# Performance work log

Hardware: AMD Instinct MI355X
Metric: run time of the kernel (lower is better)

## Reference

```python
import jax, jax.numpy as jnp
import numpy as np

N_SAMPLES = 10
DROPOUT_P = 0.1
EPS = 1e-12
B, F, C = 32768, 512, 1000


def setup_inputs() -> dict:
    key = jax.random.key(0)
    k1, k2, k3, k4 = jax.random.split(key, 4)
    return {
        "features": jax.random.normal(k1, (B, F), dtype=jnp.float32),
        "logits": jax.random.normal(k2, (B, C), dtype=jnp.float32),
        "W": jax.random.normal(k3, (F, C), dtype=jnp.float32) * 0.05,
        "b": jax.random.normal(k4, (C,), dtype=jnp.float32) * 0.05,
    }


def reference(features, logits, W, b):
    # `logits` is part of the provider interface but unused by this provider.
    del logits
    keep_p = 1.0 - DROPOUT_P
    mask_key = jax.random.key(42)
    # (n_samples, batch, feat) Bernoulli keep masks; inverted-dropout scaling.
    masks = jax.random.bernoulli(mask_key, keep_p, (N_SAMPLES,) + features.shape)
    dropped = jnp.where(masks, features[None] / keep_p, 0.0)  # (S, B, F)
    lgts = jnp.einsum("sbf,fc->sbc", dropped, W) + b          # (S, B, C)
    probs = jax.nn.softmax(lgts, axis=-1)                      # (S, B, C)
    mean = jnp.mean(probs, axis=0)                             # (B, C)
    # torch .var(dim=0) uses unbiased (n-1) normalization.
    var = jnp.sum((probs - mean[None]) ** 2, axis=0) / (N_SAMPLES - 1)
    total_var = jnp.sum(var, axis=-1, keepdims=True)           # (B, 1)
    # Scaler not fitted -> _normalize is identity.
    return jnp.log(total_var + EPS)
```

## Files before the change

kernel.cpp:

```cpp
#include <hip/hip_runtime.h>
#include <hip/hip_bf16.h>
#include <stdint.h>
#include <math.h>

typedef __attribute__((ext_vector_type(8))) short short8;
typedef __attribute__((ext_vector_type(4))) float f32x4;

namespace {
constexpr int kB = 32768;
constexpr int kF = 512;
constexpr int kC = 1000;
constexpr int kCpad = 1024;
constexpr int kS = 10;
constexpr int G = 8;
constexpr int M = G * kS;
constexpr int MT = M / 16;
constexpr int NTW = 8;
constexpr int WAVES = 8;
constexpr int SK = 64;
constexpr int SLICES = kF / SK;
constexpr uint32_t SLICE_BYTES = M * SK * 2;
}

__device__ __forceinline__ uint32_t rotl32(uint32_t x, uint32_t r) {
  return (x << r) | (x >> (32u - r));
}

__device__ __forceinline__ uint32_t threefry2x32_xor(uint32_t c0, uint32_t c1) {
  const uint32_t ks0 = 0u;
  const uint32_t ks1 = 42u;
  const uint32_t ks2 = 0x1BD11BDAu ^ ks0 ^ ks1;
  uint32_t x0 = c0 + ks0;
  uint32_t x1 = c1 + ks1;
#define TF_ROUND(r) { x0 += x1; x1 = rotl32(x1, r); x1 ^= x0; }
  TF_ROUND(13u) TF_ROUND(15u) TF_ROUND(26u) TF_ROUND(6u)
  x0 += ks1; x1 += ks2 + 1u;
  TF_ROUND(17u) TF_ROUND(29u) TF_ROUND(16u) TF_ROUND(24u)
  x0 += ks2; x1 += ks0 + 2u;
  TF_ROUND(13u) TF_ROUND(15u) TF_ROUND(26u) TF_ROUND(6u)
  x0 += ks0; x1 += ks1 + 3u;
  TF_ROUND(17u) TF_ROUND(29u) TF_ROUND(16u) TF_ROUND(24u)
  x0 += ks1; x1 += ks2 + 4u;
  TF_ROUND(13u) TF_ROUND(15u) TF_ROUND(26u) TF_ROUND(6u)
  x0 += ks2; x1 += ks0 + 5u;
#undef TF_ROUND
  return x0 ^ x1;
}

__device__ __forceinline__ uint32_t f2bf(float x) {
  uint32_t u = __float_as_uint(x);
  return (u + 0x7fffu + ((u >> 16) & 1u)) >> 16;
}

__device__ __forceinline__ uint32_t pack_bf16x2(float lo, float hi) {
  __hip_bfloat162 h = __float22bfloat162_rn(make_float2(lo, hi));
  return *reinterpret_cast<uint32_t*>(&h);
}


__global__ __launch_bounds__(256) void prep_wt(const float* __restrict__ W,
                                               ushort* __restrict__ Wt) {
  __shared__ float tile[64][65];
  const int kt = blockIdx.x * 64;
  const int ct = blockIdx.y * 64;
  const int tid = threadIdx.x;
#pragma unroll
  for (int i = 0; i < 16; ++i) {
    const int lin = i * 256 + tid;
    const int rk = lin >> 6, cc = lin & 63;
    const int gc = ct + cc;
    tile[rk][cc] = (gc < kC) ? W[(size_t)(kt + rk) * kC + gc] : 0.0f;
  }
  __syncthreads();
#pragma unroll
  for (int i = 0; i < 8; ++i) {
    const int lin = i * 256 + tid;
    const int cc = lin >> 5, kp = lin & 31;
    const int gc = ct + cc;
    const uint32_t lo = f2bf(tile[kp * 2][cc]);
    const uint32_t hi = f2bf(tile[kp * 2 + 1][cc]);
    ((uint32_t*)Wt)[(size_t)gc * (kF / 2) + (kt >> 1) + kp] = lo | (hi << 16);
  }
}

__global__ __launch_bounds__(256) void prep_bias(const float* __restrict__ b,
                                                 float* __restrict__ biasp) {
  const int i = blockIdx.x * 256 + threadIdx.x;
  if (i < kCpad) biasp[i] = (i < kC) ? b[i] : -INFINITY;
}


__global__ __launch_bounds__(512, 2) void mc_mfma_kernel(
    const float* __restrict__ features, const ushort* __restrict__ Wt,
    const float* __restrict__ biasp, float* __restrict__ out) {
  __shared__ __align__(16) ushort Abuf[2][M * SK];
  __shared__ float wred[M][9];
  __shared__ float rowinv[M];
  __shared__ float part[G][9];

  const int tid = threadIdx.x;
  const int b0 = blockIdx.x * G;
  const int wv = tid >> 6;
  const int lane = tid & 63;
  const int cp = lane & 15;
  const int gr = lane >> 4;
  const int cbase = wv * 128;

  const int fp = tid & 31;
  const int mbase = tid >> 5;
  const int gg = mbase & 7;
  const int s0 = mbase >> 3;
  char* const Ab0 = (char*)&Abuf[0][0];

  auto gen_slice = [&](int sl, uint32_t lbase) {
    const uint32_t fo =
        (uint32_t)(b0 + gg) * kF + (uint32_t)(sl * SK + fp * 2);
    const float2 fv = *(const float2*)(features + fo);
    const float f0 = fv.x * (1.0f / 0.9f);
    const float f1 = fv.y * (1.0f / 0.9f);
    uint32_t idx = (uint32_t)s0 * (uint32_t)(kB * kF) + fo;
    const uint32_t byte0 =
        lbase + (((uint32_t)(mbase * 128 + fp * 4)) ^ ((uint32_t)gg << 4));
#pragma unroll
    for (int i = 0; i < 5; ++i) {
      const uint32_t bits0 = threefry2x32_xor(0u, idx);
      const uint32_t bits1 = threefry2x32_xor(0u, idx + 1u);
      const float a0 = ((bits0 >> 9) < 7549747u) ? f0 : 0.0f;
      const float a1 = ((bits1 >> 9) < 7549747u) ? f1 : 0.0f;
      *(uint32_t*)(Ab0 + byte0 + (uint32_t)i * 2048u) = pack_bf16x2(a0, a1);
      idx += (1u << 25);
    }
  };

  f32x4 acc[MT][NTW];
#pragma unroll
  for (int mt = 0; mt < MT; ++mt)
#pragma unroll
    for (int nt = 0; nt < NTW; ++nt)
#pragma unroll
      for (int r = 0; r < 4; ++r) acc[mt][nt][r] = 0.0f;

  const uint32_t wbase = (uint32_t)(cbase + cp) * kF + (uint32_t)(gr * 8);
  const uint32_t aswz = (uint32_t)((cp & 7) << 4);
  const uint32_t arow = (uint32_t)(cp * 128);

  gen_slice(0, 0u);
  __syncthreads();

#pragma unroll 2
  for (int sl = 0; sl < SLICES; ++sl) {
    const uint32_t cur = (uint32_t)(sl & 1) * SLICE_BYTES;
    const uint32_t nxt = cur ^ SLICE_BYTES;
    const uint32_t wsl = wbase + (uint32_t)(sl * SK);

    short8 bf[NTW];
#pragma unroll
    for (int nt = 0; nt < NTW; ++nt)
      bf[nt] = *(const short8*)(Wt + wsl + (uint32_t)nt * 8192u);

    if (sl + 1 < SLICES) gen_slice(sl + 1, nxt);

    {
      const char* Ar = (const char*)Ab0 + cur;
      short8 a[MT];
#pragma unroll
      for (int mt = 0; mt < MT; ++mt)
        a[mt] = *(const short8*)(Ar + (uint32_t)(mt * 2048) + arow +
                                 (((uint32_t)(gr * 16)) ^ aswz));
      __builtin_amdgcn_s_setprio(1);
#pragma unroll
      for (int nt = 0; nt < NTW; ++nt)
#pragma unroll
        for (int mt = 0; mt < MT; ++mt)
          acc[mt][nt] = __builtin_amdgcn_mfma_f32_16x16x32_bf16(
              a[mt], bf[nt], acc[mt][nt], 0, 0, 0);
      __builtin_amdgcn_s_setprio(0);
    }

#pragma unroll
    for (int nt = 0; nt < NTW; ++nt)
      bf[nt] = *(const short8*)(Wt + wsl + 32u + (uint32_t)nt * 8192u);

    {
      const char* Ar = (const char*)Ab0 + cur;
      short8 a[MT];
#pragma unroll
      for (int mt = 0; mt < MT; ++mt)
        a[mt] = *(const short8*)(Ar + (uint32_t)(mt * 2048) + arow +
                                 (((uint32_t)(64 + gr * 16)) ^ aswz));
      __builtin_amdgcn_s_setprio(1);
#pragma unroll
      for (int nt = 0; nt < NTW; ++nt)
#pragma unroll
        for (int mt = 0; mt < MT; ++mt)
          acc[mt][nt] = __builtin_amdgcn_mfma_f32_16x16x32_bf16(
              a[mt], bf[nt], acc[mt][nt], 0, 0, 0);
      __builtin_amdgcn_s_setprio(0);
    }
    __syncthreads();
  }

  const float* bp = biasp + cbase + cp;
  float bias_lane[NTW];
#pragma unroll
  for (int nt = 0; nt < NTW; ++nt) bias_lane[nt] = bp[nt * 16];

  float red[MT][4];
#pragma unroll
  for (int mt = 0; mt < MT; ++mt)
#pragma unroll
    for (int r = 0; r < 4; ++r) {
      float z = 0.0f;
#pragma unroll
      for (int nt = 0; nt < NTW; ++nt) {
        const float e = __expf(acc[mt][nt][r] + bias_lane[nt]);
        acc[mt][nt][r] = e;
        z += e;
      }
      red[mt][r] = z;
    }
#pragma unroll
  for (int off = 1; off <= 8; off <<= 1)
#pragma unroll
    for (int mt = 0; mt < MT; ++mt)
#pragma unroll
      for (int r = 0; r < 4; ++r) red[mt][r] += __shfl_xor(red[mt][r], off);
  if (cp == 0) {
#pragma unroll
    for (int mt = 0; mt < MT; ++mt)
#pragma unroll
      for (int r = 0; r < 4; ++r) wred[mt * 16 + gr * 4 + r][wv] = red[mt][r];
  }
  __syncthreads();
  if (tid < M) {
    float z = 0.0f;
#pragma unroll
    for (int w = 0; w < WAVES; ++w) z += wred[tid][w];
    rowinv[tid] = 1.0f / z;
  }
  __syncthreads();

#pragma unroll
  for (int mt = 0; mt < MT; ++mt)
#pragma unroll
    for (int r = 0; r < 4; ++r) red[mt][r] = rowinv[mt * 16 + gr * 4 + r];

  float vp[4] = {0.0f, 0.0f, 0.0f, 0.0f};
#pragma unroll
  for (int nt = 0; nt < NTW; ++nt)
#pragma unroll
    for (int r = 0; r < 4; ++r) {
      float sp = 0.0f, sp2 = 0.0f;
#pragma unroll
      for (int mt = 0; mt < MT; ++mt) {
        const float p = acc[mt][nt][r] * red[mt][r];
        sp += p;
        sp2 += p * p;
      }
      sp += __shfl_xor(sp, 32);
      sp2 += __shfl_xor(sp2, 32);
      vp[r] += sp2 - sp * sp * 0.1f;
    }
#pragma unroll
  for (int off = 1; off <= 8; off <<= 1)
#pragma unroll
    for (int r = 0; r < 4; ++r) vp[r] += __shfl_xor(vp[r], off);
  if (cp == 0 && gr < 2) {
#pragma unroll
    for (int r = 0; r < 4; ++r) part[gr * 4 + r][wv] = vp[r];
  }
  __syncthreads();
  if (tid < G) {
    float t = 0.0f;
#pragma unroll
    for (int w = 0; w < WAVES; ++w) t += part[tid][w];
    t = fmaxf(t, 0.0f);
    out[b0 + tid] = logf(t * (1.0f / 9.0f) + 1e-12f);
  }
}


template <bool IS_MAX>
__device__ __forceinline__ float block_reduce(float v, float* red) {
#pragma unroll
  for (int off = 32; off >= 1; off >>= 1) {
    const float o = __shfl_xor(v, off);
    v = IS_MAX ? fmaxf(v, o) : (v + o);
  }
  const int wid = threadIdx.x >> 6;
  if ((threadIdx.x & 63) == 0) red[wid] = v;
  __syncthreads();
  float r = red[0];
#pragma unroll
  for (int w = 1; w < 4; ++w) r = IS_MAX ? fmaxf(r, red[w]) : (r + red[w]);
  __syncthreads();
  return r;
}

__global__ __launch_bounds__(256) void mc_dropout_var_kernel(
    const float* __restrict__ features, const float* __restrict__ W,
    const float* __restrict__ bias, float* __restrict__ out) {
  const int b = blockIdx.x;
  const int tid = threadIdx.x;
  __shared__ float mf[kS][kF];
  __shared__ float red[4];
  const uint32_t row_base = (uint32_t)b * (uint32_t)kF;
  for (int k = 0; k < (kS * kF) / 256; ++k) {
    const int lin = k * 256 + tid;
    const int s = lin >> 9;
    const int f = lin & (kF - 1);
    const uint32_t idx =
        (uint32_t)s * (uint32_t)(kB * kF) + row_base + (uint32_t)f;
    const uint32_t bits = threefry2x32_xor(0u, idx);
    const float u = __uint_as_float((bits >> 9) | 0x3f800000u) - 1.0f;
    const float fv = features[row_base + f];
    mf[s][f] = (u < 0.9f) ? (fv / 0.9f) : 0.0f;
  }
  __syncthreads();
  const bool active = (tid < kC / 4);
  const int c0 = tid * 4;
  float acc[kS][4];
#pragma unroll
  for (int s = 0; s < kS; ++s)
#pragma unroll
    for (int j = 0; j < 4; ++j) acc[s][j] = 0.0f;
  if (active) {
    const float* wp = W + c0;
    for (int f = 0; f < kF; f += 4) {
      float wv[4][4];
      *reinterpret_cast<float4*>(wv[0]) =
          *reinterpret_cast<const float4*>(wp + (size_t)(f + 0) * kC);
      *reinterpret_cast<float4*>(wv[1]) =
          *reinterpret_cast<const float4*>(wp + (size_t)(f + 1) * kC);
      *reinterpret_cast<float4*>(wv[2]) =
          *reinterpret_cast<const float4*>(wp + (size_t)(f + 2) * kC);
      *reinterpret_cast<float4*>(wv[3]) =
          *reinterpret_cast<const float4*>(wp + (size_t)(f + 3) * kC);
#pragma unroll
      for (int s = 0; s < kS; ++s) {
        float mm[4];
        *reinterpret_cast<float4*>(mm) =
            *reinterpret_cast<const float4*>(&mf[s][f]);
#pragma unroll
        for (int j = 0; j < 4; ++j) {
#pragma unroll
          for (int q = 0; q < 4; ++q)
            acc[s][j] = fmaf(mm[q], wv[q][j], acc[s][j]);
        }
      }
    }
  }
  float bias_r[4] = {0.f, 0.f, 0.f, 0.f};
  if (active) {
    const float4 bb = *reinterpret_cast<const float4*>(bias + c0);
    bias_r[0] = bb.x; bias_r[1] = bb.y; bias_r[2] = bb.z; bias_r[3] = bb.w;
  }
  float sum_p[4] = {0.f, 0.f, 0.f, 0.f};
  float sum_p2[4] = {0.f, 0.f, 0.f, 0.f};
#pragma unroll 1
  for (int s = 0; s < kS; ++s) {
    float l[4] = {0.f, 0.f, 0.f, 0.f};
    float lmax = -INFINITY;
    if (active) {
#pragma unroll
      for (int j = 0; j < 4; ++j) {
        l[j] = acc[s][j] + bias_r[j];
        lmax = fmaxf(lmax, l[j]);
      }
    }
    const float bmax = block_reduce<true>(lmax, red);
    float psum = 0.f;
    float p[4] = {0.f, 0.f, 0.f, 0.f};
    if (active) {
#pragma unroll
      for (int j = 0; j < 4; ++j) {
        p[j] = expf(l[j] - bmax);
        psum += p[j];
      }
    }
    const float bsum = block_reduce<false>(psum, red);
    const float inv = 1.0f / bsum;
    if (active) {
#pragma unroll
      for (int j = 0; j < 4; ++j) {
        const float pr = p[j] * inv;
        sum_p[j] += pr;
        sum_p2[j] += pr * pr;
      }
    }
  }
  float partv = 0.f;
  if (active) {
#pragma unroll
    for (int j = 0; j < 4; ++j)
      partv += (sum_p2[j] - sum_p[j] * sum_p[j] * 0.1f) * (1.0f / 9.0f);
  }
  const float total = block_reduce<false>(partv, red);
  if (tid == 0) out[b] = logf(total + 1e-12f);
}


extern "C" void kernel_launch(void* const* d_in, const int* in_sizes, int n_in,
                              void* d_out, int out_size, void* d_ws, size_t ws_size,
                              hipStream_t stream) {
  const float* features = (const float*)d_in[0];
  const float* W = (const float*)d_in[2];
  const float* bias = (const float*)d_in[3];
  float* out = (float*)d_out;

  const size_t wt_bytes = (size_t)kCpad * kF * sizeof(ushort);
  const size_t need = wt_bytes + (size_t)kCpad * sizeof(float);

  if (ws_size >= need) {
    ushort* Wt = (ushort*)d_ws;
    float* biasp = (float*)((char*)d_ws + wt_bytes);
    hipLaunchKernelGGL(prep_wt, dim3(kF / 64, kCpad / 64), dim3(256), 0, stream,
                       W, Wt);
    hipLaunchKernelGGL(prep_bias, dim3((kCpad + 255) / 256), dim3(256), 0,
                       stream, bias, biasp);
    hipLaunchKernelGGL(mc_mfma_kernel, dim3(kB / G), dim3(512), 0, stream,
                       features, Wt, biasp, out);
  } else {
    hipLaunchKernelGGL(mc_dropout_var_kernel, dim3(kB), dim3(256), 0, stream,
                       features, W, bias, out);
  }
}
```

Before: 820.7 us.

## Precompute dropout masks via ballot and stage full A matrix in LDS

Replaces the double-buffered per-slice generation of the dropped-feature A tile, which was interleaved with the MFMA loop, with a separate prologue. The prologue first computes all Threefry keep bits into ballot bitmasks in shared memory, then builds the whole 80x512 bf16 A matrix in LDS, and only then runs a sync-free K loop over that resident matrix. This is meant to remove the per-slice barriers and the mixing of RNG ALU work with matrix work. The cost is losing the overlap between RNG and MFMA, plus a much larger LDS footprint (about 85 KB per block), which likely stops two blocks from fitting per CU. It also switches to a rotate builtin and an inline v_cvt_pk_bf16_f32 for bf16 packing.

New measurement: 913.3 us. 1.11x slower.

```diff
diff --git a/kernel.cpp b/kernel.cpp
--- a/kernel.cpp
+++ b/kernel.cpp
@@ -17,13 +17,15 @@
 constexpr int MT = M / 16;
 constexpr int NTW = 8;
 constexpr int WAVES = 8;
-constexpr int SK = 64;
-constexpr int SLICES = kF / SK;
-constexpr uint32_t SLICE_BYTES = M * SK * 2;
+constexpr uint32_t kKeepThr = 3865470464u;
 }
 
 __device__ __forceinline__ uint32_t rotl32(uint32_t x, uint32_t r) {
+#if __has_builtin(__builtin_rotateleft32)
+  return __builtin_rotateleft32(x, r);
+#else
   return (x << r) | (x >> (32u - r));
+#endif
 }
 
 __device__ __forceinline__ uint32_t threefry2x32_xor(uint32_t c0, uint32_t c1) {
@@ -53,8 +55,9 @@
 }
 
 __device__ __forceinline__ uint32_t pack_bf16x2(float lo, float hi) {
-  __hip_bfloat162 h = __float22bfloat162_rn(make_float2(lo, hi));
-  return *reinterpret_cast<uint32_t*>(&h);
+  uint32_t r;
+  asm("v_cvt_pk_bf16_f32 %0, %1, %2" : "=v"(r) : "v"(lo), "v"(hi));
+  return r;
 }
 
 
@@ -93,7 +96,8 @@
 __global__ __launch_bounds__(512, 2) void mc_mfma_kernel(
     const float* __restrict__ features, const ushort* __restrict__ Wt,
     const float* __restrict__ biasp, float* __restrict__ out) {
-  __shared__ __align__(16) ushort Abuf[2][M * SK];
+  __shared__ __align__(16) ushort A_sh[M * kF];
+  __shared__ uint64_t mask64[M][WAVES];
   __shared__ float wred[M][9];
   __shared__ float rowinv[M];
   __shared__ float part[G][9];
@@ -105,32 +109,49 @@
   const int cp = lane & 15;
   const int gr = lane >> 4;
   const int cbase = wv * 128;
-
-  const int fp = tid & 31;
-  const int mbase = tid >> 5;
-  const int gg = mbase & 7;
-  const int s0 = mbase >> 3;
-  char* const Ab0 = (char*)&Abuf[0][0];
-
-  auto gen_slice = [&](int sl, uint32_t lbase) {
-    const uint32_t fo =
-        (uint32_t)(b0 + gg) * kF + (uint32_t)(sl * SK + fp * 2);
-    const float2 fv = *(const float2*)(features + fo);
-    const float f0 = fv.x * (1.0f / 0.9f);
-    const float f1 = fv.y * (1.0f / 0.9f);
-    uint32_t idx = (uint32_t)s0 * (uint32_t)(kB * kF) + fo;
-    const uint32_t byte0 =
-        lbase + (((uint32_t)(mbase * 128 + fp * 4)) ^ ((uint32_t)gg << 4));
-#pragma unroll
-    for (int i = 0; i < 5; ++i) {
-      const uint32_t bits0 = threefry2x32_xor(0u, idx);
-      const uint32_t bits1 = threefry2x32_xor(0u, idx + 1u);
-      const float a0 = ((bits0 >> 9) < 7549747u) ? f0 : 0.0f;
-      const float a1 = ((bits1 >> 9) < 7549747u) ? f1 : 0.0f;
-      *(uint32_t*)(Ab0 + byte0 + (uint32_t)i * 2048u) = pack_bf16x2(a0, a1);
-      idx += (1u << 25);
-    }
-  };
+  char* const Ab0 = (char*)A_sh;
+
+  {
+    const uint32_t fcol = (uint32_t)(wv * 64 + lane);
+#pragma unroll 2
+    for (int t = 0; t < M; ++t) {
+      const uint32_t idx = ((uint32_t)(t >> 3) << 24) +
+                           (uint32_t)(b0 + (t & 7)) * (uint32_t)kF + fcol;
+      const uint32_t bits = threefry2x32_xor(0u, idx);
+      const unsigned long long bal = __ballot(bits < kKeepThr);
+      if (lane == 0) mask64[t][wv] = bal;
+    }
+  }
+  __syncthreads();
+
+  {
+    const int fp = tid & 31;
+    const int mbase = tid >> 5;
+    const int gg = mbase & 7;
+    const uint32_t* mask32 = (const uint32_t*)&mask64[0][0];
+    const float2* const fbase =
+        (const float2*)features + ((uint32_t)(b0 + gg) * (kF / 2) + fp);
+    const uint32_t swzw = (uint32_t)gg << 4;
+    const uint32_t sh = (uint32_t)((fp * 2) & 31);
+    const uint32_t msel = (uint32_t)(fp >> 4);
+#pragma unroll
+    for (int j = 0; j < 8; ++j) {
+      const float2 fv = fbase[j * 32];
+      const float f0 = fv.x * (1.0f / 0.9f);
+      const float f1 = fv.y * (1.0f / 0.9f);
+#pragma unroll
+      for (int i = 0; i < 5; ++i) {
+        const int m = mbase + 16 * i;
+        const uint32_t mw = mask32[m * 16 + j * 2 + msel];
+        const float a0 = ((mw >> sh) & 1u) ? f0 : 0.0f;
+        const float a1 = ((mw >> sh) & 2u) ? f1 : 0.0f;
+        *(uint32_t*)(Ab0 +
+                     (((uint32_t)(m * 1024 + j * 128 + fp * 4)) ^ swzw)) =
+            pack_bf16x2(a0, a1);
+      }
+    }
+  }
+  __syncthreads();
 
   f32x4 acc[MT][NTW];
 #pragma unroll
@@ -142,62 +163,29 @@
 
   const uint32_t wbase = (uint32_t)(cbase + cp) * kF + (uint32_t)(gr * 8);
   const uint32_t aswz = (uint32_t)((cp & 7) << 4);
-  const uint32_t arow = (uint32_t)(cp * 128);
-
-  gen_slice(0, 0u);
-  __syncthreads();
-
-#pragma unroll 2
-  for (int sl = 0; sl < SLICES; ++sl) {
-    const uint32_t cur = (uint32_t)(sl & 1) * SLICE_BYTES;
-    const uint32_t nxt = cur ^ SLICE_BYTES;
-    const uint32_t wsl = wbase + (uint32_t)(sl * SK);
-
+  const uint32_t arow = (uint32_t)(cp * 1024);
+
+#pragma unroll 1
+  for (int ks = 0; ks < kF / 32; ++ks) {
     short8 bf[NTW];
 #pragma unroll
     for (int nt = 0; nt < NTW; ++nt)
-      bf[nt] = *(const short8*)(Wt + wsl + (uint32_t)nt * 8192u);
-
-    if (sl + 1 < SLICES) gen_slice(sl + 1, nxt);
-
-    {
-      const char* Ar = (const char*)Ab0 + cur;
-      short8 a[MT];
+      bf[nt] = *(const short8*)(Wt + wbase + (uint32_t)(ks * 32) +
+                                (uint32_t)nt * 8192u);
+    short8 a[MT];
+    const uint32_t koff = ((uint32_t)(ks * 64 + gr * 16)) ^ aswz;
+#pragma unroll
+    for (int mt = 0; mt < MT; ++mt)
+      a[mt] = *(const short8*)(Ab0 + arow + (uint32_t)(mt * 16384) + koff);
+
+    __builtin_amdgcn_s_setprio(1);
+#pragma unroll
+    for (int nt = 0; nt < NTW; ++nt)
 #pragma unroll
       for (int mt = 0; mt < MT; ++mt)
-        a[mt] = *(const short8*)(Ar + (uint32_t)(mt * 2048) + arow +
-                                 (((uint32_t)(gr * 16)) ^ aswz));
-      __builtin_amdgcn_s_setprio(1);
-#pragma unroll
-      for (int nt = 0; nt < NTW; ++nt)
-#pragma unroll
-        for (int mt = 0; mt < MT; ++mt)
-          acc[mt][nt] = __builtin_amdgcn_mfma_f32_16x16x32_bf16(
-              a[mt], bf[nt], acc[mt][nt], 0, 0, 0);
-      __builtin_amdgcn_s_setprio(0);
-    }
-
-#pragma unroll
-    for (int nt = 0; nt < NTW; ++nt)
-      bf[nt] = *(const short8*)(Wt + wsl + 32u + (uint32_t)nt * 8192u);
-
-    {
-      const char* Ar = (const char*)Ab0 + cur;
-      short8 a[MT];
-#pragma unroll
-      for (int mt = 0; mt < MT; ++mt)
-        a[mt] = *(const short8*)(Ar + (uint32_t)(mt * 2048) + arow +
-                                 (((uint32_t)(64 + gr * 16)) ^ aswz));
-      __builtin_amdgcn_s_setprio(1);
-#pragma unroll
-      for (int nt = 0; nt < NTW; ++nt)
-#pragma unroll
-        for (int mt = 0; mt < MT; ++mt)
-          acc[mt][nt] = __builtin_amdgcn_mfma_f32_16x16x32_bf16(
-              a[mt], bf[nt], acc[mt][nt], 0, 0, 0);
-      __builtin_amdgcn_s_setprio(0);
-    }
-    __syncthreads();
+        acc[mt][nt] = __builtin_amdgcn_mfma_f32_16x16x32_bf16(
+            a[mt], bf[nt], acc[mt][nt], 0, 0, 0);
+    __builtin_amdgcn_s_setprio(0);
   }
 
   const float* bp = biasp + cbase + cp;
```
